# Kernel optimization log

Hardware: AMD Instinct MI355X
Metric: run time of the kernel (lower is better)

## Reference

```python
import jax, jax.numpy as jnp
import numpy as np
import math

DIM = 512
BLOCK_NUM = 16
SEQ_LEN = 8192
BLOCK_LEN = SEQ_LEN // BLOCK_NUM  # 512 == DIM -> mask used as-is
BATCH = 4
LN_EPS = 1e-3  # keras LayerNormalization default epsilon


def setup_inputs() -> dict:
    key = jax.random.key(0)
    ks = jax.random.split(key, 5)
    inputs = jax.random.normal(ks[0], (BATCH, BLOCK_NUM, BLOCK_LEN, DIM), dtype=jnp.float32)
    # binary padding-style mask, values in {0,1}
    mask_array = jax.random.randint(ks[1], (BATCH, SEQ_LEN, DIM), 0, 2).astype(jnp.float32)
    scale = 1.0 / math.sqrt(DIM)
    dw1 = jax.random.normal(ks[2], (DIM, DIM), dtype=jnp.float32) * scale
    dw2 = jax.random.normal(ks[3], (DIM, DIM), dtype=jnp.float32) * scale
    dw3 = jax.random.normal(ks[4], (DIM, DIM), dtype=jnp.float32) * scale
    db1 = jnp.zeros((DIM,), dtype=jnp.float32)
    db2 = jnp.zeros((DIM,), dtype=jnp.float32)
    db3 = jnp.zeros((DIM,), dtype=jnp.float32)
    return {"inputs": inputs, "mask_array": mask_array,
            "dw1": dw1, "dw2": dw2, "dw3": dw3,
            "db1": db1, "db2": db2, "db3": db3}


def reference(inputs, mask_array, dw1, dw2, dw3, db1, db2, db3):
    # inputs: [B, block_num, block_len, dim]
    Q = jnp.matmul(inputs, dw1) + db1
    K = jnp.matmul(inputs, dw2) + db2
    V = jnpp_matmul = jnp.matmul(inputs, dw3) + db3
    V = jnp.matmul(inputs, dw3) + db3
    # block-local attention scores: [B, bn, bl, bl]
    scores = jnp.einsum('bnqd,bnkd->bnqk', Q, K) / math.sqrt(DIM)
    # mask: [B, seq_len, dim] -> [B, bn, bl, dim]; block_len == dim so no slice/tile
    m = mask_array.reshape(BATCH, BLOCK_NUM, BLOCK_LEN, DIM)
    scores = scores + (1.0 - m) * jnp.float32(-1e10)
    p = jax.nn.softmax(scores, axis=-1)
    out = jnp.einsum('bnqk,bnkd->bnqd', p, V) + inputs  # residual
    # LayerNorm(axis=-1), fresh keras layer: gamma=1, beta=0, eps=1e-3
    mean = jnp.mean(out, axis=-1, keepdims=True)
    var = jnp.mean(jnp.square(out - mean), axis=-1, keepdims=True)
    return (out - mean) / jnp.sqrt(var + LN_EPS)
```

## Files before the change

kernel.cpp:

```cpp
#include <hip/hip_runtime.h>

#define DIMK 512
#define NBLK 64
#define NTOK 32768

typedef short  short8 __attribute__((ext_vector_type(8)));
typedef float  f32x4  __attribute__((ext_vector_type(4)));
typedef unsigned short u16x8 __attribute__((ext_vector_type(8)));

__device__ __forceinline__ unsigned short f2bf(float f) {
  union { float f; unsigned u; } v; v.f = f;
  unsigned r = (v.u + 0x7FFFu + ((v.u >> 16) & 1u)) >> 16;
  return (unsigned short)r;
}
__device__ __forceinline__ float bf2f(unsigned short h) {
  return __uint_as_float(((unsigned)h) << 16);
}

__device__ __forceinline__ void gload_lds16(const unsigned short* g,
                                            unsigned short* l) {
  __builtin_amdgcn_global_load_lds(
      (const __attribute__((address_space(1))) unsigned int*)(g),
      (__attribute__((address_space(3))) unsigned int*)(l),
      16, 0, 0);
}

__device__ __forceinline__ int swz(int c) { return c ^ ((c >> 3) & 3); }


__global__ __launch_bounds__(256) void k_prep(
    const float* __restrict__ X, const float* __restrict__ mask,
    const float* __restrict__ dw1, const float* __restrict__ dw2,
    const float* __restrict__ dw3,
    unsigned short* __restrict__ Xb, unsigned char* __restrict__ bits,
    unsigned short* __restrict__ Wt)
{
  __shared__ __align__(16) unsigned short sbuf[32 * 520];
  const int b = blockIdx.x;
  const int tid = threadIdx.x;
  if (b < 1024) {
    const size_t t0 = (size_t)b * 32;
#pragma unroll
    for (int r = 0; r < 8; ++r) {
      const int idx = r * 256 + tid;
      const int tl = idx >> 6;
      const int col = (idx & 63) * 8;
      const float4 a = *(const float4*)&X[(t0 + tl) * 512 + col];
      const float4 c = *(const float4*)&X[(t0 + tl) * 512 + col + 4];
      u16x8 o;
      o[0] = f2bf(a.x); o[1] = f2bf(a.y); o[2] = f2bf(a.z); o[3] = f2bf(a.w);
      o[4] = f2bf(c.x); o[5] = f2bf(c.y); o[6] = f2bf(c.z); o[7] = f2bf(c.w);
      *(u16x8*)&sbuf[tl * 520 + col] = o;
    }
    __syncthreads();
    const int trow = b >> 2;
    const int srow = (b & 3) * 32;
#pragma unroll
    for (int r = 0; r < 8; ++r) {
      const int c = r * 256 + tid;
      const int kt = c >> 7;
      const int cc = c & 127;
      const int tl = cc >> 2, kko = (cc & 3) * 8;
      *(u16x8*)&Xb[((size_t)trow * 16 + kt) * 4096 + (srow + tl) * 32 + kko] =
          *(const u16x8*)&sbuf[tl * 520 + kt * 32 + kko];
    }
  } else if (b < 9216) {
    const size_t gid = (size_t)(b - 1024) * 256 + tid;
    const size_t i = gid * 8;
    const float4 ma = *(const float4*)(mask + i);
    const float4 mb = *(const float4*)(mask + i + 4);
    unsigned v = 0;
    v |= (ma.x > 0.5f) << 0; v |= (ma.y > 0.5f) << 1;
    v |= (ma.z > 0.5f) << 2; v |= (ma.w > 0.5f) << 3;
    v |= (mb.x > 0.5f) << 4; v |= (mb.y > 0.5f) << 5;
    v |= (mb.z > 0.5f) << 6; v |= (mb.w > 0.5f) << 7;
    bits[gid] = (unsigned char)v;
  } else {
    float (*t)[65] = (float(*)[65])sbuf;
    const int bb = b - 9216;
    const int w = bb >> 6;
    const int tt = bb & 63;
    const int kt = (tt >> 3) * 64;
    const int nt = (tt & 7) * 64;
    const float* dw = (w == 0) ? dw1 : (w == 1) ? dw2 : dw3;
    const int rr = tid >> 4;
    const int cc = (tid & 15) << 2;
#pragma unroll
    for (int p = 0; p < 4; ++p) {
      const int r = rr + p * 16;
      const float4 v = *(const float4*)&dw[(size_t)(kt + r) * 512 + nt + cc];
      t[cc + 0][r] = v.x; t[cc + 1][r] = v.y;
      t[cc + 2][r] = v.z; t[cc + 3][r] = v.w;
    }
    __syncthreads();
#pragma unroll
    for (int p = 0; p < 4; ++p) {
      const int r = rr + p * 16;
      const int n = nt + r;
      const int k = kt + cc;
      ushort4 o;
      o.x = f2bf(t[r][cc + 0]); o.y = f2bf(t[r][cc + 1]);
      o.z = f2bf(t[r][cc + 2]); o.w = f2bf(t[r][cc + 3]);
      *(ushort4*)&Wt[(size_t)w * 262144 + (size_t)(k >> 5) * 16384 +
                     (size_t)n * 32 + (k & 31)] = o;
    }
  }
}

__global__ __launch_bounds__(256, 2) void k_qkv(
    const unsigned short* __restrict__ Xb, const unsigned short* __restrict__ Wt,
    const float* __restrict__ db1, const float* __restrict__ db2,
    const float* __restrict__ db3,
    unsigned short* __restrict__ Qb, unsigned short* __restrict__ Kb,
    unsigned short* __restrict__ Vt)
{
  __shared__ __align__(16) unsigned short smem[32768];

  const int id = blockIdx.x;
  const int x = id & 7, j = id >> 3;
  const int mtile = x * 32 + (j >> 2);
  const int nt = j & 3;
  const int m0 = mtile * 128;
  const int n0 = nt * 128;

  const int tid = threadIdx.x, lane = tid & 63, wv = tid >> 6;
  const int quad = lane >> 4, l16 = lane & 15;
  const int qx = quad ^ ((l16 >> 1) & 3);
  const int rb = (wv >> 1) * 64, cb = (wv & 1) * 64;

  f32x4 acc[3][4][4];
#pragma unroll
  for (int w = 0; w < 3; ++w)
#pragma unroll
    for (int i = 0; i < 4; ++i)
#pragma unroll
      for (int jj = 0; jj < 4; ++jj) {
        f32x4 z = {0.f, 0.f, 0.f, 0.f}; acc[w][i][jj] = z;
      }

  auto stage = [&](unsigned short* base, int it) {
    const unsigned short* aslab = Xb + ((size_t)mtile * 16 + it) * 4096;
    gload_lds16(aslab + swz(tid) * 8, base + tid * 8);
    gload_lds16(aslab + swz(tid + 256) * 8, base + (tid + 256) * 8);
#pragma unroll
    for (int h = 0; h < 6; ++h) {
      const int c = tid + h * 256;
      const int w = c >> 9, cc = c & 511;
      const unsigned short* bslab =
          Wt + (size_t)w * 262144 + (size_t)it * 16384 + (size_t)n0 * 32;
      gload_lds16(bslab + swz(cc) * 8, base + 4096 + w * 4096 + cc * 8);
    }
  };

  stage(smem, 0);
  __syncthreads();
  int cur = 0;
  for (int it = 0; it < 16; ++it) {
    unsigned short* cbuf = smem + cur * 16384;
    if (it < 15) stage(smem + (cur ^ 1) * 16384, it + 1);
    const unsigned short* As = cbuf;
    const unsigned short* Bs = cbuf + 4096;
    short8 af[4];
#pragma unroll
    for (int i = 0; i < 4; ++i)
      af[i] = *(const short8*)&As[(rb + i * 16 + l16) * 32 + qx * 8];
#pragma unroll
    for (int jj = 0; jj < 4; ++jj)
#pragma unroll
      for (int w = 0; w < 3; ++w) {
        const short8 bf =
            *(const short8*)&Bs[w * 4096 + (cb + jj * 16 + l16) * 32 + qx * 8];
#pragma unroll
        for (int i = 0; i < 4; ++i)
          acc[w][i][jj] = __builtin_amdgcn_mfma_f32_16x16x32_bf16(
              af[i], bf, acc[w][i][jj], 0, 0, 0);
      }
    __syncthreads();
    cur ^= 1;
  }

#pragma unroll
  for (int i = 0; i < 4; ++i)
#pragma unroll
    for (int jj = 0; jj < 4; ++jj)
#pragma unroll
      for (int r = 0; r < 4; ++r) {
        const int tok = m0 + rb + i * 16 + quad * 4 + r;
        const int col = n0 + cb + jj * 16 + l16;
        Qb[((size_t)(tok >> 6) * 16 + (col >> 5)) * 2048 +
           (tok & 63) * 32 + (col & 31)] = f2bf(acc[0][i][jj][r] + db1[col]);
        Kb[((size_t)(tok >> 9) * 16 + (col >> 5)) * 16384 +
           (tok & 511) * 32 + (col & 31)] = f2bf(acc[1][i][jj][r] + db2[col]);
      }
#pragma unroll
  for (int i = 0; i < 4; ++i)
#pragma unroll
    for (int jj = 0; jj < 4; ++jj) {
      const int cl = cb + jj * 16 + l16;
      const int t0 = rb + i * 16 + quad * 4;
      const float bv = db3[n0 + cl];
      ushort4 pk;
      pk.x = f2bf(acc[2][i][jj][0] + bv);
      pk.y = f2bf(acc[2][i][jj][1] + bv);
      pk.z = f2bf(acc[2][i][jj][2] + bv);
      pk.w = f2bf(acc[2][i][jj][3] + bv);
      *(ushort4*)&smem[cl * 136 + t0] = pk;
    }
  __syncthreads();
#pragma unroll
  for (int h = 0; h < 8; ++h) {
    const int c = tid + h * 256;
    const int cl = c >> 4, toff = (c & 15) * 8;
    const int tg = mtile * 128 + toff;
    *(u16x8*)&Vt[(size_t)(tg >> 5) * 16384 + (size_t)(n0 + cl) * 32 +
                 (tg & 31)] = *(const u16x8*)&smem[cl * 136 + toff];
  }
}

__global__ __launch_bounds__(256, 2) void k_attn_p(
    const unsigned short* __restrict__ Qb, const unsigned short* __restrict__ Kb,
    const unsigned long long* __restrict__ bits, unsigned short* __restrict__ Pb)
{
  __shared__ __align__(16) unsigned short smem[36864];
  __shared__ float red[4][64];
  const int tid = threadIdx.x, lane = tid & 63, wv = tid >> 6;
  const int quad = lane >> 4, l16 = lane & 15;
  const int qx = quad ^ ((l16 >> 1) & 3);
  const int id = blockIdx.x;
  const int blk = (id & 7) * 8 + ((id >> 3) & 7);
  const int mt = id >> 6;
  const size_t q0 = (size_t)blk * 512 + (size_t)mt * 64;
  const int qt = blk * 8 + mt;

  f32x4 acc[4][8];
#pragma unroll
  for (int i = 0; i < 4; ++i)
#pragma unroll
    for (int j = 0; j < 8; ++j) { f32x4 z = {0.f, 0.f, 0.f, 0.f}; acc[i][j] = z; }

  auto stage = [&](unsigned short* base, int it) {
    const unsigned short* aslab = Qb + ((size_t)qt * 16 + it) * 2048;
    gload_lds16(aslab + swz(tid) * 8, base + tid * 8);
    const unsigned short* bslab = Kb + ((size_t)blk * 16 + it) * 16384;
#pragma unroll
    for (int h = 0; h < 8; ++h) {
      const int c = tid + h * 256;
      gload_lds16(bslab + swz(c) * 8, base + 2048 + c * 8);
    }
  };

  stage(smem, 0);
  __syncthreads();
  int cur = 0;
  for (int it = 0; it < 16; ++it) {
    unsigned short* cbuf = smem + cur * 18432;
    if (it < 15) stage(smem + (cur ^ 1) * 18432, it + 1);
    const unsigned short* As = cbuf;
    const unsigned short* Bs = cbuf + 2048;
    short8 af[4], bfv[8];
#pragma unroll
    for (int i = 0; i < 4; ++i)
      af[i] = *(const short8*)&As[(i * 16 + l16) * 32 + qx * 8];
#pragma unroll
    for (int j = 0; j < 8; ++j)
      bfv[j] = *(const short8*)&Bs[(wv * 128 + j * 16 + l16) * 32 + qx * 8];
#pragma unroll
    for (int i = 0; i < 4; ++i)
#pragma unroll
      for (int j = 0; j < 8; ++j)
        acc[i][j] = __builtin_amdgcn_mfma_f32_16x16x32_bf16(
            af[i], bfv[j], acc[i][j], 0, 0, 0);
    __syncthreads();
    cur ^= 1;
  }

  const float scale = 0.04419417382415922f;
  float rmax[4][4];
#pragma unroll
  for (int i = 0; i < 4; ++i)
#pragma unroll
    for (int r = 0; r < 4; ++r) rmax[i][r] = -3.0e38f;
#pragma unroll
  for (int i = 0; i < 4; ++i)
#pragma unroll
    for (int r = 0; r < 4; ++r) {
      const size_t tok = q0 + i * 16 + quad * 4 + r;
      const unsigned long long w0 = bits[tok * 8 + wv * 2];
      const unsigned long long w1 = bits[tok * 8 + wv * 2 + 1];
#pragma unroll
      for (int j = 0; j < 8; ++j) {
        const unsigned long long sel = (j < 4) ? w0 : w1;
        const float bias = ((sel >> (l16 + 16 * (j & 3))) & 1ull) ? 0.0f : -1e10f;
        const float v = acc[i][j][r] * scale + bias;
        acc[i][j][r] = v;
        rmax[i][r] = fmaxf(rmax[i][r], v);
      }
    }
#pragma unroll
  for (int i = 0; i < 4; ++i)
#pragma unroll
    for (int r = 0; r < 4; ++r)
      for (int d = 1; d < 16; d <<= 1)
        rmax[i][r] = fmaxf(rmax[i][r], __shfl_xor(rmax[i][r], d, 64));
  if (l16 == 0)
#pragma unroll
    for (int i = 0; i < 4; ++i)
#pragma unroll
      for (int r = 0; r < 4; ++r) red[wv][i * 16 + quad * 4 + r] = rmax[i][r];
  __syncthreads();
#pragma unroll
  for (int i = 0; i < 4; ++i)
#pragma unroll
    for (int r = 0; r < 4; ++r) {
      const int row = i * 16 + quad * 4 + r;
      rmax[i][r] = fmaxf(fmaxf(red[0][row], red[1][row]),
                         fmaxf(red[2][row], red[3][row]));
    }
  __syncthreads();
  float rsum[4][4];
#pragma unroll
  for (int i = 0; i < 4; ++i)
#pragma unroll
    for (int r = 0; r < 4; ++r) rsum[i][r] = 0.f;
#pragma unroll
  for (int i = 0; i < 4; ++i)
#pragma unroll
    for (int j = 0; j < 8; ++j)
#pragma unroll
      for (int r = 0; r < 4; ++r) {
        const float e = __expf(acc[i][j][r] - rmax[i][r]);
        acc[i][j][r] = e;
        rsum[i][r] += e;
      }
#pragma unroll
  for (int i = 0; i < 4; ++i)
#pragma unroll
    for (int r = 0; r < 4; ++r)
      for (int d = 1; d < 16; d <<= 1)
        rsum[i][r] += __shfl_xor(rsum[i][r], d, 64);
  if (l16 == 0)
#pragma unroll
    for (int i = 0; i < 4; ++i)
#pragma unroll
      for (int r = 0; r < 4; ++r) red[wv][i * 16 + quad * 4 + r] = rsum[i][r];
  __syncthreads();
#pragma unroll
  for (int i = 0; i < 4; ++i)
#pragma unroll
    for (int r = 0; r < 4; ++r) {
      const int row = i * 16 + quad * 4 + r;
      rsum[i][r] = 1.0f / (red[0][row] + red[1][row] + red[2][row] + red[3][row]);
    }
#pragma unroll
  for (int i = 0; i < 4; ++i)
#pragma unroll
    for (int j = 0; j < 8; ++j) {
      const int cl = wv * 128 + j * 16 + l16;
      const int t0 = i * 16 + quad * 4;
#pragma unroll
      for (int r = 0; r < 4; ++r)
        smem[(t0 + r) * 520 + cl] = f2bf(acc[i][j][r] * rsum[i][r]);
    }
  __syncthreads();
#pragma unroll
  for (int h = 0; h < 16; ++h) {
    const int c = tid + h * 256;
    const int tl = c >> 6, c0 = (c & 63) * 8;
    const int tokg = (int)q0 + tl;
    const u16x8 v = *(const u16x8*)&smem[tl * 520 + c0];
    *(u16x8*)&Pb[((size_t)(tokg >> 6) * 16 + (c0 >> 5)) * 2048 +
                 (tokg & 63) * 32 + (c0 & 31)] = v;
  }
}

__global__ __launch_bounds__(256, 2) void k_pv_ln(
    const unsigned short* __restrict__ Pb, const unsigned short* __restrict__ Vt,
    const unsigned short* __restrict__ Xb, float* __restrict__ Out)
{
  __shared__ __align__(16) unsigned short smem[36864];
  __shared__ float2 red[4][64];
  const int tid = threadIdx.x, lane = tid & 63, wv = tid >> 6;
  const int quad = lane >> 4, l16 = lane & 15;
  const int qx = quad ^ ((l16 >> 1) & 3);
  const int id = blockIdx.x;
  const int blk = (id & 7) * 8 + ((id >> 3) & 7);
  const int mt = id >> 6;
  const size_t q0 = (size_t)blk * 512 + (size_t)mt * 64;
  const int qt = blk * 8 + mt;

  f32x4 acc[4][8];
#pragma unroll
  for (int i = 0; i < 4; ++i)
#pragma unroll
    for (int j = 0; j < 8; ++j) { f32x4 z = {0.f, 0.f, 0.f, 0.f}; acc[i][j] = z; }

  auto stage = [&](unsigned short* base, int it) {
    const unsigned short* aslab = Pb + ((size_t)qt * 16 + it) * 2048;
    gload_lds16(aslab + swz(tid) * 8, base + tid * 8);
    const unsigned short* bslab = Vt + ((size_t)blk * 16 + it) * 16384;
#pragma unroll
    for (int h = 0; h < 8; ++h) {
      const int c = tid + h * 256;
      gload_lds16(bslab + swz(c) * 8, base + 2048 + c * 8);
    }
  };

  stage(smem, 0);
  __syncthreads();
  int cur = 0;
  for (int it = 0; it < 16; ++it) {
    unsigned short* cbuf = smem + cur * 18432;
    if (it < 15) stage(smem + (cur ^ 1) * 18432, it + 1);
    const unsigned short* As = cbuf;
    const unsigned short* Bs = cbuf + 2048;
    short8 af[4], bfv[8];
#pragma unroll
    for (int i = 0; i < 4; ++i)
      af[i] = *(const short8*)&As[(i * 16 + l16) * 32 + qx * 8];
#pragma unroll
    for (int j = 0; j < 8; ++j)
      bfv[j] = *(const short8*)&Bs[(wv * 128 + j * 16 + l16) * 32 + qx * 8];
#pragma unroll
    for (int i = 0; i < 4; ++i)
#pragma unroll
      for (int j = 0; j < 8; ++j)
        acc[i][j] = __builtin_amdgcn_mfma_f32_16x16x32_bf16(
            af[i], bfv[j], acc[i][j], 0, 0, 0);
    __syncthreads();
    cur ^= 1;
  }

  float vsum[4][4], vsq[4][4];
#pragma unroll
  for (int i = 0; i < 4; ++i)
#pragma unroll
    for (int r = 0; r < 4; ++r) { vsum[i][r] = 0.f; vsq[i][r] = 0.f; }
#pragma unroll
  for (int i = 0; i < 4; ++i)
#pragma unroll
    for (int j = 0; j < 8; ++j)
#pragma unroll
      for (int r = 0; r < 4; ++r) {
        const int tok = (int)(q0 + i * 16 + quad * 4 + r);
        const int col = wv * 128 + j * 16 + l16;
        const float v = acc[i][j][r] +
            bf2f(Xb[((size_t)(tok >> 7) * 16 + (col >> 5)) * 4096 +
                    (tok & 127) * 32 + (col & 31)]);
        acc[i][j][r] = v;
        vsum[i][r] += v;
        vsq[i][r] += v * v;
      }
#pragma unroll
  for (int i = 0; i < 4; ++i)
#pragma unroll
    for (int r = 0; r < 4; ++r)
      for (int d = 1; d < 16; d <<= 1) {
        vsum[i][r] += __shfl_xor(vsum[i][r], d, 64);
        vsq[i][r]  += __shfl_xor(vsq[i][r], d, 64);
      }
  if (l16 == 0)
#pragma unroll
    for (int i = 0; i < 4; ++i)
#pragma unroll
      for (int r = 0; r < 4; ++r) {
        float2 p; p.x = vsum[i][r]; p.y = vsq[i][r];
        red[wv][i * 16 + quad * 4 + r] = p;
      }
  __syncthreads();
#pragma unroll
  for (int i = 0; i < 4; ++i)
#pragma unroll
    for (int r = 0; r < 4; ++r) {
      const int row = i * 16 + quad * 4 + r;
      float s = 0.f, q = 0.f;
#pragma unroll
      for (int w = 0; w < 4; ++w) { s += red[w][row].x; q += red[w][row].y; }
      const float mean = s * (1.0f / 512.0f);
      const float var  = q * (1.0f / 512.0f) - mean * mean;
      vsum[i][r] = mean;
      vsq[i][r]  = rsqrtf(var + 1e-3f);
    }
  float* L = (float*)smem;
#pragma unroll
  for (int p = 0; p < 2; ++p) {
    __syncthreads();
    if ((wv >> 1) == p) {
#pragma unroll
      for (int i = 0; i < 4; ++i)
#pragma unroll
        for (int j = 0; j < 8; ++j) {
          const int cl = (wv & 1) * 128 + j * 16 + l16;
          const int t0 = i * 16 + quad * 4;
#pragma unroll
          for (int r = 0; r < 4; ++r)
            L[(t0 + r) * 260 + cl] = (acc[i][j][r] - vsum[i][r]) * vsq[i][r];
        }
    }
    __syncthreads();
#pragma unroll
    for (int h = 0; h < 16; ++h) {
      const int c = tid + h * 256;
      const int tl = c >> 6, c0 = (c & 63) * 4;
      const float4 v = *(const float4*)&L[tl * 260 + c0];
      *(float4*)&Out[(q0 + tl) * (size_t)DIMK + p * 256 + c0] = v;
    }
  }
}

extern "C" void kernel_launch(void* const* d_in, const int* in_sizes, int n_in,
                              void* d_out, int out_size, void* d_ws, size_t ws_size,
                              hipStream_t stream)
{
  const float* X    = (const float*)d_in[0];
  const float* mask = (const float*)d_in[1];
  const float* dw1  = (const float*)d_in[2];
  const float* dw2  = (const float*)d_in[3];
  const float* dw3  = (const float*)d_in[4];
  const float* db1  = (const float*)d_in[5];
  const float* db2  = (const float*)d_in[6];
  const float* db3  = (const float*)d_in[7];
  float* Out = (float*)d_out;

  char* ws = (char*)d_ws;
  const size_t MB = 1ull << 20;
  unsigned short* Wt = (unsigned short*)(ws);
  unsigned short* Qb = (unsigned short*)(ws + 2 * MB);
  unsigned short* Kb = (unsigned short*)(ws + 34 * MB);
  unsigned short* Vt = (unsigned short*)(ws + 66 * MB);
  unsigned short* Xb = (unsigned short*)(ws + 98 * MB);
  unsigned short* Pb = Qb;
  unsigned char*  bits = (unsigned char*)d_out;

  k_prep   <<<9408, 256, 0, stream>>>(X, mask, dw1, dw2, dw3, Xb, bits, Wt);
  k_qkv    <<<1024, 256, 0, stream>>>(Xb, Wt, db1, db2, db3, Qb, Kb, Vt);
  k_attn_p <<<512, 256, 0, stream>>>(Qb, Kb, (const unsigned long long*)bits, Pb);
  k_pv_ln  <<<512, 256, 0, stream>>>(Pb, Vt, Xb, Out);
}
```

Measured before the change: 293.5 us.

## Fuse QK softmax and PV+LayerNorm into one kernel, read float mask directly

```diff
diff --git a/kernel.cpp b/kernel.cpp
--- a/kernel.cpp
+++ b/kernel.cpp
@@ -29,11 +29,10 @@
 
 
 __global__ __launch_bounds__(256) void k_prep(
-    const float* __restrict__ X, const float* __restrict__ mask,
+    const float* __restrict__ X,
     const float* __restrict__ dw1, const float* __restrict__ dw2,
     const float* __restrict__ dw3,
-    unsigned short* __restrict__ Xb, unsigned char* __restrict__ bits,
-    unsigned short* __restrict__ Wt)
+    unsigned short* __restrict__ Xb, unsigned short* __restrict__ Wt)
 {
   __shared__ __align__(16) unsigned short sbuf[32 * 520];
   const int b = blockIdx.x;
@@ -64,20 +63,9 @@
       *(u16x8*)&Xb[((size_t)trow * 16 + kt) * 4096 + (srow + tl) * 32 + kko] =
           *(const u16x8*)&sbuf[tl * 520 + kt * 32 + kko];
     }
-  } else if (b < 9216) {
-    const size_t gid = (size_t)(b - 1024) * 256 + tid;
-    const size_t i = gid * 8;
-    const float4 ma = *(const float4*)(mask + i);
-    const float4 mb = *(const float4*)(mask + i + 4);
-    unsigned v = 0;
-    v |= (ma.x > 0.5f) << 0; v |= (ma.y > 0.5f) << 1;
-    v |= (ma.z > 0.5f) << 2; v |= (ma.w > 0.5f) << 3;
-    v |= (mb.x > 0.5f) << 4; v |= (mb.y > 0.5f) << 5;
-    v |= (mb.z > 0.5f) << 6; v |= (mb.w > 0.5f) << 7;
-    bits[gid] = (unsigned char)v;
   } else {
     float (*t)[65] = (float(*)[65])sbuf;
-    const int bb = b - 9216;
+    const int bb = b - 1024;
     const int w = bb >> 6;
     const int tt = bb & 63;
     const int kt = (tt >> 3) * 64;
@@ -217,12 +205,14 @@
   }
 }
 
-__global__ __launch_bounds__(256, 2) void k_attn_p(
+__global__ __launch_bounds__(256, 2) void k_attn_fused(
     const unsigned short* __restrict__ Qb, const unsigned short* __restrict__ Kb,
-    const unsigned long long* __restrict__ bits, unsigned short* __restrict__ Pb)
+    const unsigned short* __restrict__ Vt, const unsigned short* __restrict__ Xb,
+    const float* __restrict__ mask, float* __restrict__ Out)
 {
   __shared__ __align__(16) unsigned short smem[36864];
-  __shared__ float red[4][64];
+  __shared__ float  redf[4][64];
+  __shared__ float2 red2[4][64];
   const int tid = threadIdx.x, lane = tid & 63, wv = tid >> 6;
   const int quad = lane >> 4, l16 = lane & 15;
   const int qx = quad ^ ((l16 >> 1) & 3);
@@ -238,7 +228,7 @@
 #pragma unroll
     for (int j = 0; j < 8; ++j) { f32x4 z = {0.f, 0.f, 0.f, 0.f}; acc[i][j] = z; }
 
-  auto stage = [&](unsigned short* base, int it) {
+  auto stageQK = [&](unsigned short* base, int it) {
     const unsigned short* aslab = Qb + ((size_t)qt * 16 + it) * 2048;
     gload_lds16(aslab + swz(tid) * 8, base + tid * 8);
     const unsigned short* bslab = Kb + ((size_t)blk * 16 + it) * 16384;
@@ -249,12 +239,12 @@
     }
   };
 
-  stage(smem, 0);
+  stageQK(smem, 0);
   __syncthreads();
   int cur = 0;
   for (int it = 0; it < 16; ++it) {
     unsigned short* cbuf = smem + cur * 18432;
-    if (it < 15) stage(smem + (cur ^ 1) * 18432, it + 1);
+    if (it < 15) stageQK(smem + (cur ^ 1) * 18432, it + 1);
     const unsigned short* As = cbuf;
     const unsigned short* Bs = cbuf + 2048;
     short8 af[4], bfv[8];
@@ -285,12 +275,11 @@
 #pragma unroll
     for (int r = 0; r < 4; ++r) {
       const size_t tok = q0 + i * 16 + quad * 4 + r;
-      const unsigned long long w0 = bits[tok * 8 + wv * 2];
-      const unsigned long long w1 = bits[tok * 8 + wv * 2 + 1];
 #pragma unroll
       for (int j = 0; j < 8; ++j) {
-        const unsigned long long sel = (j < 4) ? w0 : w1;
-        const float bias = ((sel >> (l16 + 16 * (j & 3))) & 1ull) ? 0.0f : -1e10f;
+        const int col = wv * 128 + j * 16 + l16;
+        const float mv = mask[tok * (size_t)DIMK + col];
+        const float bias = (mv > 0.5f) ? 0.0f : -1e10f;
         const float v = acc[i][j][r] * scale + bias;
         acc[i][j][r] = v;
         rmax[i][r] = fmaxf(rmax[i][r], v);
@@ -306,15 +295,15 @@
 #pragma unroll
     for (int i = 0; i < 4; ++i)
 #pragma unroll
-      for (int r = 0; r < 4; ++r) red[wv][i * 16 + quad * 4 + r] = rmax[i][r];
+      for (int r = 0; r < 4; ++r) redf[wv][i * 16 + quad * 4 + r] = rmax[i][r];
   __syncthreads();
 #pragma unroll
   for (int i = 0; i < 4; ++i)
 #pragma unroll
     for (int r = 0; r < 4; ++r) {
       const int row = i * 16 + quad * 4 + r;
-      rmax[i][r] = fmaxf(fmaxf(red[0][row], red[1][row]),
-                         fmaxf(red[2][row], red[3][row]));
+      rmax[i][r] = fmaxf(fmaxf(redf[0][row], redf[1][row]),
+                         fmaxf(redf[2][row], redf[3][row]));
     }
   __syncthreads();
   float rsum[4][4];
@@ -342,61 +331,35 @@
 #pragma unroll
     for (int i = 0; i < 4; ++i)
 #pragma unroll
-      for (int r = 0; r < 4; ++r) red[wv][i * 16 + quad * 4 + r] = rsum[i][r];
+      for (int r = 0; r < 4; ++r) redf[wv][i * 16 + quad * 4 + r] = rsum[i][r];
   __syncthreads();
 #pragma unroll
   for (int i = 0; i < 4; ++i)
 #pragma unroll
     for (int r = 0; r < 4; ++r) {
       const int row = i * 16 + quad * 4 + r;
-      rsum[i][r] = 1.0f / (red[0][row] + red[1][row] + red[2][row] + red[3][row]);
-    }
+      rsum[i][r] = 1.0f / (redf[0][row] + redf[1][row] +
+                           redf[2][row] + redf[3][row]);
+    }
+
+  unsigned p16[4][8][2];
 #pragma unroll
   for (int i = 0; i < 4; ++i)
 #pragma unroll
     for (int j = 0; j < 8; ++j) {
-      const int cl = wv * 128 + j * 16 + l16;
-      const int t0 = i * 16 + quad * 4;
-#pragma unroll
-      for (int r = 0; r < 4; ++r)
-        smem[(t0 + r) * 520 + cl] = f2bf(acc[i][j][r] * rsum[i][r]);
-    }
-  __syncthreads();
-#pragma unroll
-  for (int h = 0; h < 16; ++h) {
-    const int c = tid + h * 256;
-    const int tl = c >> 6, c0 = (c & 63) * 8;
-    const int tokg = (int)q0 + tl;
-    const u16x8 v = *(const u16x8*)&smem[tl * 520 + c0];
-    *(u16x8*)&Pb[((size_t)(tokg >> 6) * 16 + (c0 >> 5)) * 2048 +
-                 (tokg & 63) * 32 + (c0 & 31)] = v;
-  }
-}
-
-__global__ __launch_bounds__(256, 2) void k_pv_ln(
-    const unsigned short* __restrict__ Pb, const unsigned short* __restrict__ Vt,
-    const unsigned short* __restrict__ Xb, float* __restrict__ Out)
-{
-  __shared__ __align__(16) unsigned short smem[36864];
-  __shared__ float2 red[4][64];
-  const int tid = threadIdx.x, lane = tid & 63, wv = tid >> 6;
-  const int quad = lane >> 4, l16 = lane & 15;
-  const int qx = quad ^ ((l16 >> 1) & 3);
-  const int id = blockIdx.x;
-  const int blk = (id & 7) * 8 + ((id >> 3) & 7);
-  const int mt = id >> 6;
-  const size_t q0 = (size_t)blk * 512 + (size_t)mt * 64;
-  const int qt = blk * 8 + mt;
-
-  f32x4 acc[4][8];
-#pragma unroll
-  for (int i = 0; i < 4; ++i)
-#pragma unroll
-    for (int j = 0; j < 8; ++j) { f32x4 z = {0.f, 0.f, 0.f, 0.f}; acc[i][j] = z; }
-
-  auto stage = [&](unsigned short* base, int it) {
-    const unsigned short* aslab = Pb + ((size_t)qt * 16 + it) * 2048;
-    gload_lds16(aslab + swz(tid) * 8, base + tid * 8);
+      p16[i][j][0] = (unsigned)f2bf(acc[i][j][0] * rsum[i][0]) |
+                     ((unsigned)f2bf(acc[i][j][1] * rsum[i][1]) << 16);
+      p16[i][j][1] = (unsigned)f2bf(acc[i][j][2] * rsum[i][2]) |
+                     ((unsigned)f2bf(acc[i][j][3] * rsum[i][3]) << 16);
+    }
+
+  f32x4 acc2[4][8];
+#pragma unroll
+  for (int i = 0; i < 4; ++i)
+#pragma unroll
+    for (int j = 0; j < 8; ++j) { f32x4 z = {0.f, 0.f, 0.f, 0.f}; acc2[i][j] = z; }
+
+  auto stageV = [&](unsigned short* base, int it) {
     const unsigned short* bslab = Vt + ((size_t)blk * 16 + it) * 16384;
 #pragma unroll
     for (int h = 0; h < 8; ++h) {
@@ -404,13 +367,37 @@
       gload_lds16(bslab + swz(c) * 8, base + 2048 + c * 8);
     }
   };
-
-  stage(smem, 0);
-  __syncthreads();
-  int cur = 0;
+  auto pubP = [&](unsigned short* base, int it) {
+    if (wv == (it >> 2)) {
+#pragma unroll
+      for (int e = 0; e < 2; ++e) {
+        const int j = (it & 3) * 2 + e;
+#pragma unroll
+        for (int i = 0; i < 4; ++i)
+#pragma unroll
+          for (int r = 0; r < 4; ++r) {
+            const int row = i * 16 + quad * 4 + r;
+            const int c = e * 16 + l16;
+            const int p = row * 4 + (((c >> 3) ^ (row >> 1)) & 3);
+            const unsigned v = p16[i][j][r >> 1];
+            base[p * 8 + (c & 7)] =
+                (unsigned short)((r & 1) ? (v >> 16) : (v & 0xFFFFu));
+          }
+      }
+    }
+  };
+
+  stageV(smem, 0);
+  pubP(smem, 0);
+  __syncthreads();
+#pragma unroll
   for (int it = 0; it < 16; ++it) {
-    unsigned short* cbuf = smem + cur * 18432;
-    if (it < 15) stage(smem + (cur ^ 1) * 18432, it + 1);
+    unsigned short* cbuf = smem + (it & 1) * 18432;
+    if (it < 15) {
+      unsigned short* nbuf = smem + ((it & 1) ^ 1) * 18432;
+      stageV(nbuf, it + 1);
+      pubP(nbuf, it + 1);
+    }
     const unsigned short* As = cbuf;
     const unsigned short* Bs = cbuf + 2048;
     short8 af[4], bfv[8];
@@ -424,10 +411,9 @@
     for (int i = 0; i < 4; ++i)
 #pragma unroll
       for (int j = 0; j < 8; ++j)
-        acc[i][j] = __builtin_amdgcn_mfma_f32_16x16x32_bf16(
-            af[i], bfv[j], acc[i][j], 0, 0, 0);
-    __syncthreads();
-    cur ^= 1;
+        acc2[i][j] = __builtin_amdgcn_mfma_f32_16x16x32_bf16(
+            af[i], bfv[j], acc2[i][j], 0, 0, 0);
+    __syncthreads();
   }
 
   float vsum[4][4], vsq[4][4];
@@ -443,10 +429,10 @@
       for (int r = 0; r < 4; ++r) {
         const int tok = (int)(q0 + i * 16 + quad * 4 + r);
         const int col = wv * 128 + j * 16 + l16;
-        const float v = acc[i][j][r] +
+        const float v = acc2[i][j][r] +
             bf2f(Xb[((size_t)(tok >> 7) * 16 + (col >> 5)) * 4096 +
                     (tok & 127) * 32 + (col & 31)]);
-        acc[i][j][r] = v;
+        acc2[i][j][r] = v;
         vsum[i][r] += v;
         vsq[i][r] += v * v;
       }
@@ -464,7 +450,7 @@
 #pragma unroll
       for (int r = 0; r < 4; ++r) {
         float2 p; p.x = vsum[i][r]; p.y = vsq[i][r];
-        red[wv][i * 16 + quad * 4 + r] = p;
+        red2[wv][i * 16 + quad * 4 + r] = p;
       }
   __syncthreads();
 #pragma unroll
@@ -474,7 +460,7 @@
       const int row = i * 16 + quad * 4 + r;
       float s = 0.f, q = 0.f;
 #pragma unroll
-      for (int w = 0; w < 4; ++w) { s += red[w][row].x; q += red[w][row].y; }
+      for (int w = 0; w < 4; ++w) { s += red2[w][row].x; q += red2[w][row].y; }
       const float mean = s * (1.0f / 512.0f);
       const float var  = q * (1.0f / 512.0f) - mean * mean;
       vsum[i][r] = mean;
@@ -493,7 +479,7 @@
           const int t0 = i * 16 + quad * 4;
 #pragma unroll
           for (int r = 0; r < 4; ++r)
-            L[(t0 + r) * 260 + cl] = (acc[i][j][r] - vsum[i][r]) * vsq[i][r];
+            L[(t0 + r) * 260 + cl] = (acc2[i][j][r] - vsum[i][r]) * vsq[i][r];
         }
     }
     __syncthreads();
@@ -528,11 +514,8 @@
   unsigned short* Kb = (unsigned short*)(ws + 34 * MB);
   unsigned short* Vt = (unsigned short*)(ws + 66 * MB);
   unsigned short* Xb = (unsigned short*)(ws + 98 * MB);
-  unsigned short* Pb = Qb;
-  unsigned char*  bits = (unsigned char*)d_out;
-
-  k_prep   <<<9408, 256, 0, stream>>>(X, mask, dw1, dw2, dw3, Xb, bits, Wt);
-  k_qkv    <<<1024, 256, 0, stream>>>(Xb, Wt, db1, db2, db3, Qb, Kb, Vt);
-  k_attn_p <<<512, 256, 0, stream>>>(Qb, Kb, (const unsigned long long*)bits, Pb);
-  k_pv_ln  <<<512, 256, 0, stream>>>(Pb, Vt, Xb, Out);
-}
+
+  k_prep       <<<1216, 256, 0, stream>>>(X, dw1, dw2, dw3, Xb, Wt);
+  k_qkv        <<<1024, 256, 0, stream>>>(Xb, Wt, db1, db2, db3, Qb, Kb, Vt);
+  k_attn_fused <<<512, 256, 0, stream>>>(Qb, Kb, Vt, Xb, mask, Out);
+}
```

After: 510.6 us. +73.9%, slower.
